# Kernel tuning notes

Hardware: AMD Instinct MI355X
Metric: run time of the kernel (lower is better)

The kernel has to match this reference:

```python
import jax, jax.numpy as jnp
import numpy as np

B, H, V, DEPTH = 64, 1024, 32000, 5


def setup_inputs() -> dict:
    key = jax.random.key(0)
    ks = jax.random.split(key, 9)
    s = 1.0 / np.sqrt(H)
    u = lambda k, shape: jax.random.uniform(k, shape, jnp.float32, -s, s)
    return {
        "encoding": jax.random.normal(ks[0], (B, H), jnp.float32),
        "Whh_l": u(ks[1], (3 * H, H)),
        "bih_l": u(ks[2], (3 * H,)),
        "bhh_l": u(ks[3], (3 * H,)),
        "Whh_r": u(ks[4], (3 * H, H)),
        "bih_r": u(ks[5], (3 * H,)),
        "bhh_r": u(ks[6], (3 * H,)),
        "W_out": u(ks[7], (V, H)),
        "b_out": u(ks[8], (V,)),
        "depth": DEPTH,
    }


def _gru_zero_input(h, Whh, bih, bhh):
    # PyTorch GRU cell with x == 0: W_ih @ x vanishes, only b_ih survives.
    d = h.shape[-1]
    gh = h @ Whh.T + bhh                                   # [N, 3H]
    r = jax.nn.sigmoid(bih[:d] + gh[..., :d])
    z = jax.nn.sigmoid(bih[d:2 * d] + gh[..., d:2 * d])
    n = jnp.tanh(bih[2 * d:] + r * gh[..., 2 * d:])
    return (1.0 - z) * n + z * h


def reference(encoding, Whh_l, bih_l, bhh_l, Whh_r, bih_r, bhh_r, W_out, b_out, depth):
    b, h = encoding.shape
    cur = encoding[:, None, :]                             # [B, 1, H] roots
    for _ in range(depth):                                 # expand perfect binary tree, level-batched
        n = cur.shape[1]
        flat = cur.reshape(b * n, h)
        left = _gru_zero_input(flat, Whh_l, bih_l, bhh_l).reshape(b, n, h)
        right = _gru_zero_input(flat, Whh_r, bih_r, bhh_r).reshape(b, n, h)
        cur = jnp.stack([left, right], axis=2).reshape(b, 2 * n, h)  # interleave children
    logits = jnp.einsum("blh,vh->blv", cur, W_out) + b_out  # [B, L, V]
    return jax.nn.log_softmax(logits, axis=-1)
```

## Files before the change

### kernel.cpp

```cpp
#include <hip/hip_runtime.h>
#include <hip/hip_bf16.h>
#include <cstdint>
#include <cstddef>

#define H_DIM   1024
#define B_DIM   64
#define V_DIM   32000
#define DEPTH_C 5

using bf16x8  = __attribute__((ext_vector_type(8))) __bf16;
using bf16x4  = __attribute__((ext_vector_type(4))) __bf16;
using floatx4 = __attribute__((ext_vector_type(4))) float;

__device__ __forceinline__ void gl_lds16(const __bf16* g, __bf16* l) {
  __builtin_amdgcn_global_load_lds(
      (const __attribute__((address_space(1))) unsigned int*)g,
      (__attribute__((address_space(3))) unsigned int*)l, 16, 0, 0);
}

__global__ __launch_bounds__(256) void f2b(const float* __restrict__ in,
                                           __bf16* __restrict__ out, int n) {
  for (int i = (blockIdx.x * 256 + threadIdx.x) * 4; i < n;
       i += gridDim.x * 1024) {
    float4 v = *(const float4*)(in + i);
    bf16x4 o;
    o[0] = (__bf16)v.x; o[1] = (__bf16)v.y; o[2] = (__bf16)v.z; o[3] = (__bf16)v.w;
    *(bf16x4*)(out + i) = o;
  }
}

__device__ __forceinline__ bf16x8 cvt8(float4 a, float4 b) {
  bf16x8 r;
  r[0] = (__bf16)a.x; r[1] = (__bf16)a.y; r[2] = (__bf16)a.z; r[3] = (__bf16)a.w;
  r[4] = (__bf16)b.x; r[5] = (__bf16)b.y; r[6] = (__bf16)b.z; r[7] = (__bf16)b.w;
  return r;
}

template <int TN, bool LOGITS, bool WBF16>
__global__ __launch_bounds__(256) void gemm_nt(
    const __bf16* __restrict__ A, const __bf16* __restrict__ Wb0,
    const __bf16* __restrict__ Wb1, const float* __restrict__ Wf,
    __bf16* __restrict__ Cb, float* __restrict__ Cf,
    const float* __restrict__ bias, float2* __restrict__ part, int M, int N) {
  constexpr int K = H_DIM;
  constexpr int MI = (TN == 128) ? 4 : 2;
  __shared__ __align__(16) __bf16 As[128 * 32];
  __shared__ __align__(16) __bf16 Bs[TN * 32];

  const int tid  = threadIdx.x;
  const int nbx = gridDim.x;
  const int nwg = nbx * gridDim.y;
  int hflat = blockIdx.y * nbx + blockIdx.x;
  if ((nwg & 7) == 0) {
    const int cpx = nwg >> 3;
    hflat = (hflat & 7) * cpx + (hflat >> 3);
  }
  const int bx = hflat % nbx;
  const int by = hflat / nbx;
  const int m0   = bx * 128;
  const int n0   = by * TN;
  const int lane = tid & 63;
  const int wave = tid >> 6;
  const int lrow = lane & 15;
  const int quad = lane >> 4;
  const int wm   = (TN == 128) ? (wave >> 1) * 64 : wave * 32;
  const int wn   = (TN == 128) ? (wave & 1) * 64 : 0;

  const __bf16* Wb = Wb0;
  int nw0 = n0;
  if (!LOGITS && n0 >= 3072) { Wb = Wb1; nw0 = n0 - 3072; }

  const int sr = tid >> 2;
  const int sk = (tid & 3) * 8;

  int ra0 = m0 + sr;      if (ra0 >= M) ra0 = M - 1;
  int ra1 = m0 + sr + 64; if (ra1 >= M) ra1 = M - 1;
  const __bf16* ga0 = A + (size_t)ra0 * K + sk;
  const __bf16* ga1 = A + (size_t)ra1 * K + sk;
  const __bf16* gb0 = nullptr; const __bf16* gb1 = nullptr;
  const float* gf0 = nullptr; const float* gf1 = nullptr;
  if (WBF16) {
    gb0 = Wb + (size_t)(nw0 + sr) * K + sk;
    if (TN == 128) gb1 = Wb + (size_t)(nw0 + sr + 64) * K + sk;
  } else {
    gf0 = Wf + (size_t)(n0 + sr) * K + sk;
    gf1 = Wf + (size_t)(n0 + sr + 64) * K + sk;
  }

  floatx4 acc[MI][4] = {};

  for (int kt = 0; kt < K; kt += 32) {
    float4 w00, w01, w10, w11;
    if (!WBF16) {
      w00 = *(const float4*)(gf0 + kt);
      w01 = *(const float4*)(gf0 + kt + 4);
      w10 = *(const float4*)(gf1 + kt);
      w11 = *(const float4*)(gf1 + kt + 4);
    }
    __syncthreads();
    gl_lds16(ga0 + kt, As + tid * 8);
    gl_lds16(ga1 + kt, As + 2048 + tid * 8);
    if (WBF16) {
      gl_lds16(gb0 + kt, Bs + tid * 8);
      if (TN == 128) gl_lds16(gb1 + kt, Bs + 2048 + tid * 8);
    } else {
      *(bf16x8*)(&Bs[sr * 32 + sk])        = cvt8(w00, w01);
      *(bf16x8*)(&Bs[(sr + 64) * 32 + sk]) = cvt8(w10, w11);
    }
    __syncthreads();

    bf16x8 af[MI], bfr[4];
#pragma unroll
    for (int i = 0; i < MI; i++)
      af[i] = *(const bf16x8*)(&As[(wm + i * 16 + lrow) * 32 + quad * 8]);
#pragma unroll
    for (int j = 0; j < 4; j++)
      bfr[j] = *(const bf16x8*)(&Bs[(wn + j * 16 + lrow) * 32 + quad * 8]);
#pragma unroll
    for (int i = 0; i < MI; i++)
#pragma unroll
      for (int j = 0; j < 4; j++)
        acc[i][j] =
            __builtin_amdgcn_mfma_f32_16x16x32_bf16(af[i], bfr[j], acc[i][j], 0, 0, 0);
  }

  float bv[4];
  if constexpr (LOGITS) {
#pragma unroll
    for (int j = 0; j < 4; j++) bv[j] = bias[n0 + wn + j * 16 + lrow];
  }
#pragma unroll
  for (int i = 0; i < MI; i++) {
#pragma unroll
    for (int j = 0; j < 4; j++) {
      const int col = n0 + wn + j * 16 + lrow;
#pragma unroll
      for (int r = 0; r < 4; r++) {
        const int row = m0 + wm + i * 16 + quad * 4 + r;
        if (row < M) {
          if (LOGITS) Cf[(size_t)row * N + col] = acc[i][j][r] + bv[j];
          else        Cb[(size_t)row * N + col] = (__bf16)acc[i][j][r];
        }
      }
    }
  }

  if constexpr (LOGITS) {
    __shared__ float pmax[2][128], psum[2][128];
    const int wnh = wn >> 6;
#pragma unroll
    for (int i = 0; i < MI; i++) {
#pragma unroll
      for (int r = 0; r < 4; r++) {
        float mx = -3.0e38f;
#pragma unroll
        for (int j = 0; j < 4; j++) mx = fmaxf(mx, acc[i][j][r] + bv[j]);
#pragma unroll
        for (int mask = 1; mask < 16; mask <<= 1)
          mx = fmaxf(mx, __shfl_xor(mx, mask, 64));
        float sm = 0.f;
#pragma unroll
        for (int j = 0; j < 4; j++) sm += __expf(acc[i][j][r] + bv[j] - mx);
#pragma unroll
        for (int mask = 1; mask < 16; mask <<= 1)
          sm += __shfl_xor(sm, mask, 64);
        if (lrow == 0) {
          pmax[wnh][wm + i * 16 + quad * 4 + r] = mx;
          psum[wnh][wm + i * 16 + quad * 4 + r] = sm;
        }
      }
    }
    __syncthreads();
    if (tid < 128) {
      const float ma = pmax[0][tid], mb = pmax[1][tid];
      const float nm = fmaxf(ma, mb);
      const float ns = psum[0][tid] * __expf(ma - nm) +
                       psum[1][tid] * __expf(mb - nm);
      part[(size_t)(m0 + tid) * gridDim.y + by] = make_float2(nm, ns);
    }
  }
}

__global__ __launch_bounds__(256) void gru_gate(
    const __bf16* __restrict__ gh, const float* __restrict__ bih_l,
    const float* __restrict__ bhh_l, const float* __restrict__ bih_r,
    const float* __restrict__ bhh_r, const __bf16* __restrict__ hin,
    __bf16* __restrict__ hout, int n) {
  const int row = blockIdx.x;
  const int col = blockIdx.y * 256 + threadIdx.x;
  const int b = row / n, j = row - b * n;
  const size_t g6 = (size_t)row * 6144;
  const float hv = (float)hin[(size_t)row * H_DIM + col];
  const size_t obase = (size_t)(b * 2 * n + 2 * j) * H_DIM;

  {
    float gr = (float)gh[g6 + col] + bhh_l[col];
    float gz = (float)gh[g6 + 1024 + col] + bhh_l[1024 + col];
    float gn = (float)gh[g6 + 2048 + col] + bhh_l[2048 + col];
    float r = 1.f / (1.f + __expf(-(bih_l[col] + gr)));
    float z = 1.f / (1.f + __expf(-(bih_l[1024 + col] + gz)));
    float nn = tanhf(bih_l[2048 + col] + r * gn);
    hout[obase + col] = (__bf16)((1.f - z) * nn + z * hv);
  }
  {
    float gr = (float)gh[g6 + 3072 + col] + bhh_r[col];
    float gz = (float)gh[g6 + 4096 + col] + bhh_r[1024 + col];
    float gn = (float)gh[g6 + 5120 + col] + bhh_r[2048 + col];
    float r = 1.f / (1.f + __expf(-(bih_r[col] + gr)));
    float z = 1.f / (1.f + __expf(-(bih_r[1024 + col] + gz)));
    float nn = tanhf(bih_r[2048 + col] + r * gn);
    hout[obase + H_DIM + col] = (__bf16)((1.f - z) * nn + z * hv);
  }
}

__global__ __launch_bounds__(256) void lsm_finish(
    float* __restrict__ out, const float2* __restrict__ part) {
  constexpr int NB = V_DIM / 128;
  const int row = blockIdx.x;
  const int tid = threadIdx.x;

  float m = -3.0e38f, s = 0.f;
  if (tid < NB) {
    const float2 p = part[(size_t)row * NB + tid];
    m = p.x; s = p.y;
  }
#pragma unroll
  for (int off = 32; off; off >>= 1) {
    float om = __shfl_xor(m, off, 64);
    float os = __shfl_xor(s, off, 64);
    float nm = fmaxf(m, om);
    s = s * __expf(m - nm) + os * __expf(om - nm);
    m = nm;
  }
  __shared__ float rm[4], rs[4];
  if ((tid & 63) == 0) { rm[tid >> 6] = m; rs[tid >> 6] = s; }
  __syncthreads();
  const float M4 = fmaxf(fmaxf(rm[0], rm[1]), fmaxf(rm[2], rm[3]));
  const float S4 = rs[0] * __expf(rm[0] - M4) + rs[1] * __expf(rm[1] - M4) +
                   rs[2] * __expf(rm[2] - M4) + rs[3] * __expf(rm[3] - M4);
  const float lg = M4 + __logf(S4);

  float4* p4 = (float4*)(out + (size_t)row * V_DIM);
  for (int i = tid; i < 8000; i += 256) {
    float4 v = p4[i];
    v.x -= lg; v.y -= lg; v.z -= lg; v.w -= lg;
    p4[i] = v;
  }
}

extern "C" void kernel_launch(void* const* d_in, const int* in_sizes, int n_in,
                              void* d_out, int out_size, void* d_ws,
                              size_t ws_size, hipStream_t stream) {
  const float* enc   = (const float*)d_in[0];
  const float* Whh_l = (const float*)d_in[1];
  const float* bih_l = (const float*)d_in[2];
  const float* bhh_l = (const float*)d_in[3];
  const float* Whh_r = (const float*)d_in[4];
  const float* bih_r = (const float*)d_in[5];
  const float* bhh_r = (const float*)d_in[6];
  const float* W_out = (const float*)d_in[7];
  const float* b_out = (const float*)d_in[8];
  float* out = (float*)d_out;

  char* ws = (char*)d_ws;
  __bf16* ghb    = (__bf16*)ws;
  __bf16* buf0   = (__bf16*)(ws + 12582912);
  __bf16* buf1   = (__bf16*)(ws + 16777216);
  __bf16* WhhB_l = (__bf16*)(ws + 20971520);
  __bf16* WhhB_r = WhhB_l + 3145728;
  __bf16* encB   = (__bf16*)(ws + 33554432);
  __bf16* WoutB  = (__bf16*)(ws + 33685504);
  float2* part   = (float2*)ghb;
  const bool big = ws_size >= (size_t)(33685504 + 65536000);

  f2b<<<256, 256, 0, stream>>>(Whh_l, WhhB_l, 3 * H_DIM * H_DIM);
  f2b<<<256, 256, 0, stream>>>(Whh_r, WhhB_r, 3 * H_DIM * H_DIM);
  f2b<<<64, 256, 0, stream>>>(enc, encB, B_DIM * H_DIM);
  if (big) f2b<<<1024, 256, 0, stream>>>(W_out, WoutB, V_DIM * H_DIM);

  const __bf16* cur = encB;
  __bf16* nxt = buf0;
  int n = 1;
  for (int d = 0; d < DEPTH_C; d++) {
    const int M = B_DIM * n;
    dim3 gg((M + 127) / 128, 6144 / 64);
    gemm_nt<64, false, true><<<gg, 256, 0, stream>>>(
        cur, WhhB_l, WhhB_r, nullptr, ghb, nullptr, nullptr, nullptr, M, 6144);
    gru_gate<<<dim3(M, 4), 256, 0, stream>>>(ghb, bih_l, bhh_l, bih_r, bhh_r,
                                             cur, nxt, n);
    cur = nxt;
    nxt = (nxt == buf0) ? buf1 : buf0;
    n *= 2;
  }

  dim3 gf(2048 / 128, V_DIM / 128);
  if (big)
    gemm_nt<128, true, true><<<gf, 256, 0, stream>>>(
        cur, WoutB, nullptr, nullptr, nullptr, out, b_out, part, 2048, V_DIM);
  else
    gemm_nt<128, true, false><<<gf, 256, 0, stream>>>(
        cur, nullptr, nullptr, W_out, nullptr, out, b_out, part, 2048, V_DIM);
  lsm_finish<<<2048, 256, 0, stream>>>(out, part);
}
```

Baseline: 776.7 us.

## Add 256x256 eight-phase pipelined MFMA kernel for logits GEMM

Replaces the 128x128-tile logits GEMM with a dedicated 512-thread kernel that computes 256x256 tiles. It streams 64-wide K slices into double-buffered, XOR-swizzled LDS via direct global-to-LDS loads, interleaved with MFMA phases and priority hints. The fused per-row max/sum partials are reduced within the block, so lsm_finish now takes a variable partial count (125 instead of 250). The aim is higher data reuse and better overlap of loads with matrix math on the dominant GEMM. In exchange it uses 128KB of LDS and heavy register pressure, which limits occupancy.

```diff
diff --git a/kernel.cpp b/kernel.cpp
--- a/kernel.cpp
+++ b/kernel.cpp
@@ -34,6 +34,161 @@
   r[0] = (__bf16)a.x; r[1] = (__bf16)a.y; r[2] = (__bf16)a.z; r[3] = (__bf16)a.w;
   r[4] = (__bf16)b.x; r[5] = (__bf16)b.y; r[6] = (__bf16)b.z; r[7] = (__bf16)b.w;
   return r;
+}
+
+#define VMCNT(n) asm volatile("s_waitcnt vmcnt(" #n ")" ::: "memory")
+#define SBAR()                                  \
+  do {                                          \
+    __builtin_amdgcn_sched_barrier(0);          \
+    __builtin_amdgcn_s_barrier();               \
+    __builtin_amdgcn_sched_barrier(0);          \
+  } while (0)
+#define LDA(MH, KS)                                                          \
+  do {                                                                       \
+    _Pragma("unroll") for (int mf = 0; mf < 4; ++mf)                         \
+        aF[mf] = *(const bf16x8*)(cb + aRow + (MH)*8192 + mf * 2048 +        \
+                                  ((KS) ? cksw1 : cksw0));                   \
+  } while (0)
+#define LDB(KS)                                                              \
+  do {                                                                       \
+    _Pragma("unroll") for (int nj = 0; nj < 4; ++nj)                         \
+        bB[nj] = *(const bf16x8*)(cb + 32768 + bRow + nj * 2048 +            \
+                                  ((KS) ? cksw1 : cksw0));                   \
+  } while (0)
+#define MM(MH)                                                               \
+  do {                                                                       \
+    __builtin_amdgcn_s_setprio(1);                                           \
+    _Pragma("unroll") for (int mf = 0; mf < 4; ++mf)                         \
+        _Pragma("unroll") for (int nj = 0; nj < 4; ++nj)                     \
+            acc[(MH)*4 + mf][nj] = __builtin_amdgcn_mfma_f32_16x16x32_bf16(  \
+                aF[mf], bB[nj], acc[(MH)*4 + mf][nj], 0, 0, 0);              \
+    __builtin_amdgcn_s_setprio(0);                                           \
+  } while (0)
+
+__global__ __launch_bounds__(512, 2) void gemm_logits_8ph(
+    const __bf16* __restrict__ A, const __bf16* __restrict__ Wb,
+    float* __restrict__ Cf, const float* __restrict__ bias,
+    float2* __restrict__ part) {
+  __shared__ __align__(16) char smem[131072];
+
+  const int tid = threadIdx.x;
+  int h = blockIdx.y * 8 + blockIdx.x;
+  h = (h & 7) * 125 + (h >> 3);
+  const int bx = h & 7, by = h >> 3;
+  const int m0 = bx * 256, n0 = by * 256;
+
+  const int lane = tid & 63, wave = tid >> 6;
+  const int wr = wave >> 2, wc = wave & 3;
+  const int lrow = lane & 15, quad = lane >> 4;
+
+  const int aRow  = (wr * 128 + lrow) * 128;
+  const int bRow  = (wc * 64 + lrow) * 128;
+  const int lsw   = (lrow & 7) << 4;
+  const int cksw0 = (quad * 16) ^ lsw;
+  const int cksw1 = (64 + quad * 16) ^ lsw;
+
+  const int t8  = tid >> 3;
+  const int cix = (tid & 7) ^ (t8 & 7);
+  const __bf16* gA00 = A + (size_t)(m0 + t8) * 1024 + cix * 8;
+  const __bf16* gA01 = A + (size_t)(m0 + 128 + t8) * 1024 + cix * 8;
+  const __bf16* gA10 = gA00 + 64 * 1024;
+  const __bf16* gA11 = gA01 + 64 * 1024;
+  const __bf16* gB00 = Wb + (size_t)(n0 + t8) * 1024 + cix * 8;
+  const __bf16* gB01 = Wb + (size_t)(n0 + 64 + t8) * 1024 + cix * 8;
+  const __bf16* gB10 = gB00 + 128 * 1024;
+  const __bf16* gB11 = gB01 + 128 * 1024;
+
+  floatx4 acc[8][4] = {};
+  bf16x8 aF[4], bB[4];
+
+  gl_lds16(gA00, (__bf16*)(smem + tid * 16));
+  gl_lds16(gA01, (__bf16*)(smem + 16384 + tid * 16));
+  gl_lds16(gB00, (__bf16*)(smem + 32768 + tid * 16));
+  gl_lds16(gB01, (__bf16*)(smem + 40960 + tid * 16));
+  gl_lds16(gB10, (__bf16*)(smem + 49152 + tid * 16));
+  gl_lds16(gB11, (__bf16*)(smem + 57344 + tid * 16));
+  gl_lds16(gA10, (__bf16*)(smem + 8192 + tid * 16));
+  gl_lds16(gA11, (__bf16*)(smem + 24576 + tid * 16));
+
+  for (int t = 0; t < 15; ++t) {
+    char* cb = smem + (t & 1) * 65536;
+    char* nb = smem + ((t & 1) ^ 1) * 65536;
+    const int ke = (t + 1) * 64;
+    VMCNT(2); SBAR();
+    LDB(0); LDA(0, 0);
+    gl_lds16(gA00 + ke, (__bf16*)(nb + tid * 16));
+    gl_lds16(gA01 + ke, (__bf16*)(nb + 16384 + tid * 16));
+    MM(0);
+    VMCNT(2); SBAR();
+    LDA(1, 0);
+    gl_lds16(gB00 + ke, (__bf16*)(nb + 32768 + tid * 16));
+    gl_lds16(gB01 + ke, (__bf16*)(nb + 40960 + tid * 16));
+    MM(1);
+    LDB(1); LDA(0, 1);
+    gl_lds16(gB10 + ke, (__bf16*)(nb + 49152 + tid * 16));
+    gl_lds16(gB11 + ke, (__bf16*)(nb + 57344 + tid * 16));
+    MM(0);
+    LDA(1, 1);
+    gl_lds16(gA10 + ke, (__bf16*)(nb + 8192 + tid * 16));
+    gl_lds16(gA11 + ke, (__bf16*)(nb + 24576 + tid * 16));
+    MM(1);
+  }
+  {
+    char* cb = smem + 65536;
+    VMCNT(0); SBAR();
+    LDB(0); LDA(0, 0); MM(0);
+    LDA(1, 0); MM(1);
+    LDB(1); LDA(0, 1); MM(0);
+    LDA(1, 1); MM(1);
+  }
+
+  float bv[4];
+#pragma unroll
+  for (int nj = 0; nj < 4; ++nj) bv[nj] = bias[n0 + wc * 64 + nj * 16 + lrow];
+
+  float* pm = (float*)smem;
+  float* ps = (float*)(smem + 4096);
+
+#pragma unroll
+  for (int mi = 0; mi < 8; ++mi) {
+    const int rowb = wr * 128 + mi * 16 + quad * 4;
+#pragma unroll
+    for (int r = 0; r < 4; ++r) {
+      const float v0 = acc[mi][0][r] + bv[0];
+      const float v1 = acc[mi][1][r] + bv[1];
+      const float v2 = acc[mi][2][r] + bv[2];
+      const float v3 = acc[mi][3][r] + bv[3];
+      const size_t rb = (size_t)(m0 + rowb + r) * V_DIM + n0 + wc * 64 + lrow;
+      Cf[rb]      = v0;
+      Cf[rb + 16] = v1;
+      Cf[rb + 32] = v2;
+      Cf[rb + 48] = v3;
+      float mx = fmaxf(fmaxf(v0, v1), fmaxf(v2, v3));
+#pragma unroll
+      for (int msk = 1; msk < 16; msk <<= 1)
+        mx = fmaxf(mx, __shfl_xor(mx, msk, 64));
+      float sm = __expf(v0 - mx) + __expf(v1 - mx) + __expf(v2 - mx) +
+                 __expf(v3 - mx);
+#pragma unroll
+      for (int msk = 1; msk < 16; msk <<= 1) sm += __shfl_xor(sm, msk, 64);
+      if (lrow == 0) {
+        pm[(rowb + r) * 4 + wc] = mx;
+        ps[(rowb + r) * 4 + wc] = sm;
+      }
+    }
+  }
+  __syncthreads();
+  if (tid < 256) {
+    float m = pm[tid * 4], s = ps[tid * 4];
+#pragma unroll
+    for (int w = 1; w < 4; ++w) {
+      const float om = pm[tid * 4 + w], os = ps[tid * 4 + w];
+      const float nm = fmaxf(m, om);
+      s = s * __expf(m - nm) + os * __expf(om - nm);
+      m = nm;
+    }
+    part[(size_t)(m0 + tid) * gridDim.y + by] = make_float2(m, s);
+  }
 }
 
 template <int TN, bool LOGITS, bool WBF16>
@@ -214,14 +369,13 @@
 }
 
 __global__ __launch_bounds__(256) void lsm_finish(
-    float* __restrict__ out, const float2* __restrict__ part) {
-  constexpr int NB = V_DIM / 128;
+    float* __restrict__ out, const float2* __restrict__ part, int nb) {
   const int row = blockIdx.x;
   const int tid = threadIdx.x;
 
   float m = -3.0e38f, s = 0.f;
-  if (tid < NB) {
-    const float2 p = part[(size_t)row * NB + tid];
+  if (tid < nb) {
+    const float2 p = part[(size_t)row * nb + tid];
     m = p.x; s = p.y;
   }
 #pragma unroll
@@ -293,12 +447,14 @@
     n *= 2;
   }
 
-  dim3 gf(2048 / 128, V_DIM / 128);
-  if (big)
-    gemm_nt<128, true, true><<<gf, 256, 0, stream>>>(
-        cur, WoutB, nullptr, nullptr, nullptr, out, b_out, part, 2048, V_DIM);
-  else
+  if (big) {
+    gemm_logits_8ph<<<dim3(8, 125), 512, 0, stream>>>(cur, WoutB, out, b_out,
+                                                      part);
+    lsm_finish<<<2048, 256, 0, stream>>>(out, part, 125);
+  } else {
+    dim3 gf(2048 / 128, V_DIM / 128);
     gemm_nt<128, true, false><<<gf, 256, 0, stream>>>(
         cur, nullptr, nullptr, W_out, nullptr, out, b_out, part, 2048, V_DIM);
-  lsm_finish<<<2048, 256, 0, stream>>>(out, part);
-}
+    lsm_finish<<<2048, 256, 0, stream>>>(out, part, 250);
+  }
+}
```

After: 736.6 us. 1.05x faster.
